# Optimization experiments

Hardware: AMD Instinct MI355X
Metric: run time of the kernel (lower is better)

The kernel has to match this reference:

```python
import jax, jax.numpy as jnp
import numpy as np

IN_F = 256
OUT_F = 256
H = 4
DH = OUT_F // H  # 64
N = 6144


def setup_inputs() -> dict:
    key = jax.random.key(0)
    ks = jax.random.split(key, 6)
    x = jax.random.normal(ks[0], (N, IN_F), dtype=jnp.float32)
    adj = jax.random.randint(ks[1], (N, N), 0, 2, dtype=jnp.int32)
    # per-head Linear(in_features, d_head): weights [H, IN_F, DH], bias [H, DH]
    W = jax.random.normal(ks[2], (H, IN_F, DH), dtype=jnp.float32) / np.sqrt(IN_F)
    Wb = jax.random.normal(ks[3], (H, DH), dtype=jnp.float32) * 0.01
    # per-head Linear(2*d_head, 1): weights [H, 2*DH], bias [H]
    A = jax.random.normal(ks[4], (H, 2 * DH), dtype=jnp.float32) / np.sqrt(2 * DH)
    Ab = jax.random.normal(ks[5], (H,), dtype=jnp.float32) * 0.01
    return {"x": x, "adj": adj, "W": W, "Wb": Wb, "A": A, "Ab": Ab}


def reference(x, adj, W, Wb, A, Ab):
    # h[h,n,d] = per-head linear projection of node features
    h = jnp.einsum("ni,hid->hnd", x, W) + Wb[:, None, :]
    a_src, a_dst = A[:, :DH], A[:, DH:]
    # score(i,j) = a_src . h_i + a_dst . h_j + b  (decomposed concat-linear)
    s_src = jnp.einsum("hnd,hd->hn", h, a_src) + Ab[:, None]  # [H, N]
    s_dst = jnp.einsum("hnd,hd->hn", h, a_dst)                # [H, N]
    scores = s_src[:, :, None] + s_dst[:, None, :]            # [H, N, N]
    # Faithful to source: non-edges get score 0.0 (not -inf) before softmax
    scores = jnp.where(adj[None, :, :] > 0, scores, 0.0)
    probs = jax.nn.softmax(scores, axis=-1)                   # row softmax
    out = jnp.einsum("hij,hjd->hid", probs, h)                # [H, N, DH]
    # concat heads along feature dim -> [N, H*DH]
    return jnp.transpose(out, (1, 0, 2)).reshape(N, H * DH)
```

## Files before the change

kernel.cpp:

```cpp
#include <hip/hip_runtime.h>
#include <stdint.h>

#define NN 6144
#define NC 576

typedef float f32x4 __attribute__((ext_vector_type(4)));
typedef __bf16 bf16x8v __attribute__((ext_vector_type(8)));

__device__ __forceinline__ unsigned short f2bf(float f) {
  unsigned u = __float_as_uint(f);
  u += 0x7FFFu + ((u >> 16) & 1u);
  return (unsigned short)(u >> 16);
}

__device__ __forceinline__ float bf2f(unsigned short s) {
  unsigned u = (unsigned)s << 16;
  return __uint_as_float(u);
}

__device__ __forceinline__ unsigned char f2e4m3(float f) {
  unsigned u = __float_as_uint(f);
  unsigned sgn = (u >> 24) & 0x80u;
  unsigned au = u & 0x7FFFFFFFu;
  if (au >= 0x43E00000u) return (unsigned char)(sgn | 0x7E);
  if (au < 0x3C800000u) {
    int q = (int)rintf(__uint_as_float(au) * 512.0f);
    return (unsigned char)(sgn | (q >= 8 ? 0x08 : q));
  }
  unsigned r = au + 0x7FFFFu + ((au >> 20) & 1u);
  int e = (int)(r >> 23) - 127;
  unsigned m = (r >> 20) & 7u;
  return (unsigned char)(sgn | ((unsigned)(e + 7) << 3) | m);
}

__device__ __forceinline__ unsigned short pack2(float a, float b) {
  return (unsigned short)f2e4m3(a) | ((unsigned short)f2e4m3(b) << 8);
}

__device__ __forceinline__ void async_load16(const void* g, void* l) {
  __builtin_amdgcn_global_load_lds(
      (__attribute__((address_space(1))) void*)(uintptr_t)g,
      (__attribute__((address_space(3))) void*)(uint32_t)(uintptr_t)l,
      16, 0, 0);
}

__global__ __launch_bounds__(256) void p0s(
    const float* __restrict__ W,
    const float* __restrict__ Aw, const float* __restrict__ Wb,
    unsigned short* __restrict__ wsw, float* __restrict__ Acat,
    float* __restrict__ T)
{
  const int bid = blockIdx.x, t = threadIdx.x;
  if (bid < 8) {
#pragma unroll
    for (int i = 0; i < 4; ++i) {
      const int e = bid * 256 + t + i * 2048;
      const int l = e & 63, kc = (e >> 6) & 7, ct = e >> 9;
      const int c = ct * 16 + (l & 15);
      const int h = c >> 6, d0 = c & 63;
      const int ks = kc * 32 + (l >> 4) * 8;
      const float* src = W + h * 16384 + ks * 64 + d0;
      unsigned uu[4];
#pragma unroll
      for (int j = 0; j < 4; ++j)
        uu[j] = (unsigned)f2bf(src[(2*j) * 64]) | ((unsigned)f2bf(src[(2*j+1) * 64]) << 16);
      *(uint4*)(wsw + (size_t)e * 8) = (uint4){uu[0], uu[1], uu[2], uu[3]};
    }
    return;
  }
  T[t] = 0.f;
  const int h = t >> 6, d = t & 63;
  Acat[t]       = Aw[h * 128 + d];
  Acat[256 + t] = Aw[h * 128 + 64 + d];
  Acat[512 + t] = Wb[t];
}

__global__ __launch_bounds__(256) void k1m(
    const float* __restrict__ x, const unsigned short* __restrict__ wsw,
    const float* __restrict__ Acat, const float* __restrict__ Ab,
    const int* __restrict__ adj, unsigned* __restrict__ bm,
    unsigned char* __restrict__ V8, float* __restrict__ e_src, float* __restrict__ T)
{
  __shared__ unsigned char lsh[16384];
  __shared__ float lt[256];
  const int t = threadIdx.x;

  if (blockIdx.x >= 192) {
    const int pb = blockIdx.x - 192;
    const int4* src = (const int4*)adj + (size_t)pb * 2048;
    unsigned char* ln = lsh;
#pragma unroll
    for (int i = 0; i < 8; ++i) {
      int4 q = src[t + i * 256];
      unsigned nib = (unsigned)q.x | ((unsigned)q.y << 1) |
                     ((unsigned)q.z << 2) | ((unsigned)q.w << 3);
      ln[t + i * 256] = (unsigned char)nib;
    }
    __syncthreads();
    const uint2 b2 = *(const uint2*)(ln + t * 8);
    unsigned pl = (b2.x | (b2.x >> 4)) & 0x00FF00FFu; pl = (pl | (pl >> 8)) & 0xFFFFu;
    unsigned ph = (b2.y | (b2.y >> 4)) & 0x00FF00FFu; ph = (ph | (ph >> 8)) & 0xFFFFu;
    bm[pb * 256 + t] = pl | (ph << 16);
    return;
  }

  const int w = t >> 6, l = t & 63;
  const int v = blockIdx.x * 4 + w;
  const int mt = v >> 1, nh = v & 1;
  const int i0 = mt * 16, c0 = nh * 128;
  const int lm = l & 15, lk = l >> 4;

  {
    unsigned short* lx = (unsigned short*)lsh;
    const float* xb = x + (size_t)(blockIdx.x * 32) * 256;
#pragma unroll
    for (int j = 0; j < 4; ++j) {
      const int e = t + j * 256;
      const int tile = e >> 9, e9 = e & 511;
      const int el = e9 & 63, kc = e9 >> 6;
      const int node = tile * 16 + (el & 15);
      const int ks = kc * 32 + (el >> 4) * 8;
      const float4* xp = (const float4*)(xb + (size_t)node * 256 + ks);
      float4 v0 = xp[0], v1 = xp[1];
      uint4 o;
      o.x = (unsigned)f2bf(v0.x) | ((unsigned)f2bf(v0.y) << 16);
      o.y = (unsigned)f2bf(v0.z) | ((unsigned)f2bf(v0.w) << 16);
      o.z = (unsigned)f2bf(v1.x) | ((unsigned)f2bf(v1.y) << 16);
      o.w = (unsigned)f2bf(v1.z) | ((unsigned)f2bf(v1.w) << 16);
      *(uint4*)(lx + (size_t)e * 8) = o;
    }
  }
  lt[t] = 0.f;
  __syncthreads();

  f32x4 acc[8];
#pragma unroll
  for (int nt = 0; nt < 8; ++nt) acc[nt] = (f32x4){0.f, 0.f, 0.f, 0.f};

  const unsigned short* ap = (const unsigned short*)lsh + (((size_t)(w >> 1)) * 512 + l) * 8;
  const unsigned short* bp = wsw + ((size_t)nh * 4096 + l) * 8;

#pragma unroll
  for (int kc = 0; kc < 8; ++kc) {
    bf16x8v a = *(const bf16x8v*)(ap + (size_t)kc * 512);
#pragma unroll
    for (int nt = 0; nt < 8; ++nt) {
      bf16x8v b = *(const bf16x8v*)(bp + ((size_t)nt * 512 + kc * 64) * 8);
      acc[nt] = __builtin_amdgcn_mfma_f32_16x16x32_bf16(a, b, acc[nt], 0, 0, 0);
    }
  }

  float asv[8], adv[8];
#pragma unroll
  for (int nt = 0; nt < 8; ++nt) {
    const int cc = c0 + nt * 16 + lm;
    const float wb = Acat[512 + cc];
#pragma unroll
    for (int rr = 0; rr < 4; ++rr) acc[nt][rr] += wb;
    asv[nt] = Acat[cc];
    adv[nt] = Acat[256 + cc];
  }

#pragma unroll
  for (int nt = 0; nt < 8; ++nt)
    atomicAdd(&lt[c0 + nt * 16 + lm], acc[nt][0] + acc[nt][1] + acc[nt][2] + acc[nt][3]);

  float ss[2][4], sd[2][4];
#pragma unroll
  for (int hl = 0; hl < 2; ++hl)
#pragma unroll
    for (int rr = 0; rr < 4; ++rr) {
      float s1 = 0.f, s2 = 0.f;
#pragma unroll
      for (int j = 0; j < 4; ++j) {
        s1 += acc[hl * 4 + j][rr] * asv[hl * 4 + j];
        s2 += acc[hl * 4 + j][rr] * adv[hl * 4 + j];
      }
      ss[hl][rr] = s1; sd[hl][rr] = s2;
    }
#pragma unroll
  for (int off = 1; off < 16; off <<= 1)
#pragma unroll
    for (int hl = 0; hl < 2; ++hl)
#pragma unroll
      for (int rr = 0; rr < 4; ++rr) {
        ss[hl][rr] += __shfl_xor(ss[hl][rr], off);
        sd[hl][rr] += __shfl_xor(sd[hl][rr], off);
      }

  float ed[2][4];
#pragma unroll
  for (int hl = 0; hl < 2; ++hl)
#pragma unroll
    for (int rr = 0; rr < 4; ++rr) ed[hl][rr] = expf(sd[hl][rr]);

  if (lm == 0) {
#pragma unroll
    for (int hl = 0; hl < 2; ++hl) {
      const int hh = nh * 2 + hl;
      const float ab = Ab[hh];
#pragma unroll
      for (int rr = 0; rr < 4; ++rr)
        e_src[(size_t)hh * NN + i0 + lk * 4 + rr] = expf(ss[hl][rr] + ab);
    }
  }

  __syncthreads();

  unsigned char* mylv = lsh + w * 4096;
#pragma unroll
  for (int nt = 0; nt < 8; ++nt) {
    const int hl = nt >> 2;
    const int d = (nt & 3) * 16 + lm;
    const int lcE = hl * 128 + d;
    const int lcP = lcE + 64;
    *(unsigned short*)(mylv + lcE * 16 + lk * 4)     = pack2(ed[hl][0] * acc[nt][0], ed[hl][1] * acc[nt][1]);
    *(unsigned short*)(mylv + lcE * 16 + lk * 4 + 2) = pack2(ed[hl][2] * acc[nt][2], ed[hl][3] * acc[nt][3]);
    *(unsigned short*)(mylv + lcP * 16 + lk * 4)     = pack2(acc[nt][0], acc[nt][1]);
    *(unsigned short*)(mylv + lcP * 16 + lk * 4 + 2) = pack2(acc[nt][2], acc[nt][3]);
  }
#pragma unroll
  for (int j = 0; j < 4; ++j) {
    const int lc = j * 64 + l;
    uint4 val = *(const uint4*)(mylv + lc * 16);
    *(uint4*)(V8 + (size_t)(nh * 256 + lc) * NN + i0) = val;
  }
  if (lm == 0) {
#pragma unroll
    for (int hl = 0; hl < 2; ++hl) {
      const int hh = nh * 2 + hl;
      unsigned char* pq = V8 + (size_t)(512 + hh) * NN + i0 + lk * 4;
      *(unsigned short*)pq       = pack2(ed[hl][0], ed[hl][1]);
      *(unsigned short*)(pq + 2) = pack2(ed[hl][2], ed[hl][3]);
    }
    if (nh == 0)
      *(unsigned*)(V8 + (size_t)516 * NN + i0 + lk * 4) = 0x38383838u;
  }

  __syncthreads();
  atomicAdd(&T[t], lt[t]);
}

__global__ __launch_bounds__(256, 3) void k2_gemm(
    const unsigned* __restrict__ bm, const unsigned char* __restrict__ V8,
    unsigned short* __restrict__ out2b, float* __restrict__ out2e, int nks)
{
  __shared__ unsigned char lB[2][144 * 128];
  const int t   = threadIdx.x;
  const int ks  = blockIdx.x / 192;
  const int r   = blockIdx.x - ks * 192;
  const int cb  = r & 3;
  const int rb  = r >> 2;
  const int krange = NN / nks;
  const int i0 = rb * 128, n0 = cb * 144, k0 = ks * krange;
  const int w = t >> 6, l = t & 63;
  const int lm = l & 15, lk = l >> 4;

  f32x4 acc[2][9];
#pragma unroll
  for (int mt = 0; mt < 2; ++mt)
#pragma unroll
    for (int nt = 0; nt < 9; ++nt) acc[mt][nt] = (f32x4){0.f, 0.f, 0.f, 0.f};

  int scol[5], sgr[5];
#pragma unroll
  for (int u = 0; u < 5; ++u) {
    const int gi = u * 256 + t;
    scol[u] = gi >> 3;
    sgr[u]  = (gi & 7) ^ (scol[u] & 7);
  }
  const int dbase4 = (1024 + (t & ~63)) * 16;

  const unsigned* gA0 = bm + (size_t)(i0 + w * 32 + lm) * (NN / 32) + (k0 >> 5) + lk;
  const unsigned char* gBb = V8 + (size_t)n0 * NN + k0;

  const int iters = krange / 128;

#define K2_STAGE(BUF, IT)                                                        \
  do {                                                                           \
    const unsigned char* gB = gBb + (IT) * 128;                                  \
    _Pragma("unroll")                                                            \
    for (int u = 0; u < 4; ++u)                                                  \
      async_load16(gB + (size_t)scol[u] * NN + sgr[u] * 16,                      \
                   (char*)lB[BUF] + (size_t)(u * 256 + (t & ~63)) * 16);         \
    if (t < 128)                                                                 \
      async_load16(gB + (size_t)scol[4] * NN + sgr[4] * 16,                      \
                   (char*)lB[BUF] + dbase4);                                     \
  } while (0)

  unsigned bits_c[2], bits_n[2];
  K2_STAGE(0, 0);
#pragma unroll
  for (int mt = 0; mt < 2; ++mt) bits_c[mt] = gA0[(size_t)mt * 16 * (NN / 32)];
  __syncthreads();

  int cur = 0;
  for (int it = 0; it < iters; ++it) {
    if (it + 1 < iters) {
      K2_STAGE(cur ^ 1, it + 1);
#pragma unroll
      for (int mt = 0; mt < 2; ++mt)
        bits_n[mt] = gA0[(size_t)mt * 16 * (NN / 32) + (it + 1) * 4];
    }

    longlong2 afr[2][2];
#pragma unroll
    for (int mt = 0; mt < 2; ++mt) {
      unsigned u[8];
#pragma unroll
      for (int i = 0; i < 8; ++i) {
        unsigned nib = (bits_c[mt] >> (4 * i)) & 0xFu;
        u[i] = ((nib * 0x00204081u) & 0x01010101u) << 3;
      }
      afr[mt][0].x = (long long)(((unsigned long long)u[1] << 32) | u[0]);
      afr[mt][0].y = (long long)(((unsigned long long)u[3] << 32) | u[2]);
      afr[mt][1].x = (long long)(((unsigned long long)u[5] << 32) | u[4]);
      afr[mt][1].y = (long long)(((unsigned long long)u[7] << 32) | u[6]);
    }

#pragma unroll
    for (int b = 0; b < 2; ++b) {
#pragma unroll
      for (int nt = 0; nt < 9; ++nt) {
        const int cc = nt * 16 + lm;
        const int pos = (lk * 2 + b) ^ (cc & 7);
        longlong2 bv = *(const longlong2*)(lB[cur] + cc * 128 + pos * 16);
#pragma unroll
        for (int mt = 0; mt < 2; ++mt) {
          acc[mt][nt] = __builtin_amdgcn_mfma_f32_16x16x32_fp8_fp8(
              afr[mt][b].x, bv.x, acc[mt][nt], 0, 0, 0);
          acc[mt][nt] = __builtin_amdgcn_mfma_f32_16x16x32_fp8_fp8(
              afr[mt][b].y, bv.y, acc[mt][nt], 0, 0, 0);
        }
      }
    }

    if (it + 1 < iters) {
#pragma unroll
      for (int mt = 0; mt < 2; ++mt) bits_c[mt] = bits_n[mt];
    }
    __syncthreads();
    cur ^= 1;
  }
#undef K2_STAGE

  unsigned short* lw = (unsigned short*)((char*)lB[0] + w * 4608);
  float* oe = out2e + (size_t)ks * ((size_t)NN * 64);
  unsigned short* pb = out2b + ((size_t)(ks * 4 + cb) * NN + i0 + w * 32) * 144;
#pragma unroll
  for (int mt = 0; mt < 2; ++mt) {
#pragma unroll
    for (int nt = 0; nt < 9; ++nt) {
      const int coll = nt * 16 + lm;
#pragma unroll
      for (int rr = 0; rr < 4; ++rr)
        lw[(lk * 4 + rr) * 144 + coll] = f2bf(acc[mt][nt][rr] * 64.0f);
      if (cb == 3 && nt >= 5) {
        const int row = i0 + w * 32 + mt * 16 + lk * 4;
#pragma unroll
        for (int rr = 0; rr < 4; ++rr)
          oe[(size_t)(row + rr) * 64 + (n0 + coll - 512)] = acc[mt][nt][rr] * 64.0f;
      }
    }
    const uint4* ls = (const uint4*)((char*)lB[0] + w * 4608);
    char* dst = (char*)(pb + (size_t)mt * 16 * 144);
    for (int s = l; s < 288; s += 64)
      *(uint4*)(dst + s * 16) = ls[s];
  }
}

__global__ __launch_bounds__(256) void k3_final(
    const unsigned short* __restrict__ out2b, const float* __restrict__ out2e,
    const float* __restrict__ e_src, const float* __restrict__ T,
    float* __restrict__ out, int nks)
{
  const int n = blockIdx.x, c = threadIdx.x;
  const int h = c >> 6, d = c & 63;
  const int cS = h * 128 + d, cP = cS + 64;
  const int cbS = cS / 144, ofS = cS % 144;
  const int cbP = cP / 144, ofP = cP % 144;
  float Se = 0.f, Sp = 0.f, E = 0.f, dg = 0.f;
  for (int s = 0; s < nks; ++s) {
    const unsigned short* base = out2b + (size_t)s * 4 * NN * 144;
    Se += bf2f(base[((size_t)cbS * NN + n) * 144 + ofS]);
    Sp += bf2f(base[((size_t)cbP * NN + n) * 144 + ofP]);
    const float* re = out2e + (size_t)s * NN * 64 + (size_t)n * 64;
    E  += re[h];
    dg += re[4];
  }
  float e = e_src[h * NN + n];
  float D = e * E + ((float)NN - dg);
  out[(size_t)n * 256 + c] = (e * Se + (T[c] - Sp)) / D;
}

extern "C" void kernel_launch(void* const* d_in, const int* in_sizes, int n_in,
                              void* d_out, int out_size, void* d_ws, size_t ws_size,
                              hipStream_t stream) {
  const float* x  = (const float*)d_in[0];
  const int*   adj= (const int*)d_in[1];
  const float* W  = (const float*)d_in[2];
  const float* Wb = (const float*)d_in[3];
  const float* Aw = (const float*)d_in[4];
  const float* Ab = (const float*)d_in[5];
  float* out = (float*)d_out;
  char* ws = (char*)d_ws;
  unsigned char* V8 = (unsigned char*)ws;
  float* e_src = (float*)(ws + 3538944);
  float* T     = (float*)(ws + 3637248);
  float* Acat  = (float*)(ws + 3638272);
  unsigned short* wsw = (unsigned short*)(ws + 3641344);
  unsigned* bm = (unsigned*)(ws + 6918144);
  unsigned short* out2b = (unsigned short*)(ws + 44666880);
  float* out2e = (float*)(ws + 87134208);

  const size_t slabB = (size_t)4 * NN * 144 * 2;
  const size_t slabE = (size_t)NN * 64 * 4;
  int nks = 2;
  if (ws_size >= 44666880 + 4 * slabB + 4 * slabE)  nks = 4;

  hipLaunchKernelGGL(p0s, dim3(9), dim3(256), 0, stream,
                     W, Aw, Wb, wsw, Acat, T);
  hipLaunchKernelGGL(k1m, dim3(4800), dim3(256), 0, stream,
                     x, wsw, Acat, Ab, adj, bm, V8, e_src, T);
  hipLaunchKernelGGL(k2_gemm, dim3(192 * nks), dim3(256), 0, stream, bm, V8, out2b, out2e, nks);
  hipLaunchKernelGGL(k3_final, dim3(NN), dim3(256), 0, stream, out2b, out2e, e_src, T, out, nks);
}
```

Before: 271.5 us.

## Split k2 GEMM loads into phases interleaved with MFMA via fine-grained waitcnt barriers

Restructures the k2_gemm main loop into three MFMA phases of three N-tiles each. The next stage's async global-to-LDS loads are issued in chunks between phases, and explicit vmcnt waits plus s_barrier replace the single per-iteration __syncthreads. s_setprio raises wave priority during MFMA bursts. The intent is to overlap load issue with compute and shorten barrier stalls. In exchange, LDS padding grows to 160 rows so all threads issue the fifth load unconditionally, which uses more shared memory and may reduce occupancy. The hand-tuned waitcnt counts are fragile.

```diff
diff --git a/kernel.cpp b/kernel.cpp
--- a/kernel.cpp
+++ b/kernel.cpp
@@ -245,7 +245,7 @@
     const unsigned* __restrict__ bm, const unsigned char* __restrict__ V8,
     unsigned short* __restrict__ out2b, float* __restrict__ out2e, int nks)
 {
-  __shared__ unsigned char lB[2][144 * 128];
+  __shared__ unsigned char lB[2][160 * 128];
   const int t   = threadIdx.x;
   const int ks  = blockIdx.x / 192;
   const int r   = blockIdx.x - ks * 192;
@@ -269,80 +269,120 @@
     scol[u] = gi >> 3;
     sgr[u]  = (gi & 7) ^ (scol[u] & 7);
   }
-  const int dbase4 = (1024 + (t & ~63)) * 16;
 
   const unsigned* gA0 = bm + (size_t)(i0 + w * 32 + lm) * (NN / 32) + (k0 >> 5) + lk;
   const unsigned char* gBb = V8 + (size_t)n0 * NN + k0;
 
   const int iters = krange / 128;
 
-#define K2_STAGE(BUF, IT)                                                        \
-  do {                                                                           \
-    const unsigned char* gB = gBb + (IT) * 128;                                  \
-    _Pragma("unroll")                                                            \
-    for (int u = 0; u < 4; ++u)                                                  \
-      async_load16(gB + (size_t)scol[u] * NN + sgr[u] * 16,                      \
-                   (char*)lB[BUF] + (size_t)(u * 256 + (t & ~63)) * 16);         \
-    if (t < 128)                                                                 \
-      async_load16(gB + (size_t)scol[4] * NN + sgr[4] * 16,                      \
-                   (char*)lB[BUF] + dbase4);                                     \
+#define K2_ISSUE(U)                                                             \
+  async_load16(gBn + (size_t)scol[U] * NN + sgr[U] * 16,                        \
+               dst + (size_t)((U) * 256 + (t & ~63)) * 16)
+
+#define K2_EXPAND                                                               \
+  do {                                                                          \
+    unsigned bits[2] = {bc0, bc1};                                              \
+    _Pragma("unroll")                                                           \
+    for (int mtq = 0; mtq < 2; ++mtq) {                                         \
+      unsigned u[8];                                                            \
+      _Pragma("unroll")                                                         \
+      for (int i = 0; i < 8; ++i) {                                             \
+        unsigned nib = (bits[mtq] >> (4 * i)) & 0xFu;                           \
+        u[i] = ((nib * 0x00204081u) & 0x01010101u) << 3;                        \
+      }                                                                         \
+      afr[mtq][0].x = (long long)(((unsigned long long)u[1] << 32) | u[0]);     \
+      afr[mtq][0].y = (long long)(((unsigned long long)u[3] << 32) | u[2]);     \
+      afr[mtq][1].x = (long long)(((unsigned long long)u[5] << 32) | u[4]);     \
+      afr[mtq][1].y = (long long)(((unsigned long long)u[7] << 32) | u[6]);     \
+    }                                                                           \
   } while (0)
 
-  unsigned bits_c[2], bits_n[2];
-  K2_STAGE(0, 0);
-#pragma unroll
-  for (int mt = 0; mt < 2; ++mt) bits_c[mt] = gA0[(size_t)mt * 16 * (NN / 32)];
+#define K2_MFMA_PHASE(NTB)                                                      \
+  __builtin_amdgcn_s_setprio(1);                                                \
+  _Pragma("unroll")                                                             \
+  for (int b2 = 0; b2 < 2; ++b2) {                                              \
+    _Pragma("unroll")                                                           \
+    for (int q = 0; q < 3; ++q) {                                               \
+      const int cc = ((NTB) + q) * 16 + lm;                                     \
+      const int pos = (lk * 2 + b2) ^ (cc & 7);                                 \
+      longlong2 bv = *(const longlong2*)(lB[cur] + cc * 128 + pos * 16);        \
+      _Pragma("unroll")                                                         \
+      for (int mtq = 0; mtq < 2; ++mtq) {                                       \
+        acc[mtq][(NTB) + q] = __builtin_amdgcn_mfma_f32_16x16x32_fp8_fp8(       \
+            afr[mtq][b2].x, bv.x, acc[mtq][(NTB) + q], 0, 0, 0);                \
+        acc[mtq][(NTB) + q] = __builtin_amdgcn_mfma_f32_16x16x32_fp8_fp8(       \
+            afr[mtq][b2].y, bv.y, acc[mtq][(NTB) + q], 0, 0, 0);                \
+      }                                                                         \
+    }                                                                           \
+  }                                                                             \
+  __builtin_amdgcn_s_setprio(0)
+
+  unsigned bc0 = gA0[0];
+  unsigned bc1 = gA0[16 * (NN / 32)];
+  {
+    const unsigned char* gBn = gBb;
+    unsigned char* dst = (unsigned char*)lB[0];
+#pragma unroll
+    for (int u = 0; u < 5; ++u) { K2_ISSUE(u); }
+  }
+  asm volatile("s_waitcnt vmcnt(0)" ::: "memory");
   __syncthreads();
 
   int cur = 0;
-  for (int it = 0; it < iters; ++it) {
-    if (it + 1 < iters) {
-      K2_STAGE(cur ^ 1, it + 1);
-#pragma unroll
-      for (int mt = 0; mt < 2; ++mt)
-        bits_n[mt] = gA0[(size_t)mt * 16 * (NN / 32) + (it + 1) * 4];
-    }
-
+  for (int it = 0; it < iters - 1; ++it) {
+    const unsigned char* gBn = gBb + (it + 1) * 128;
+    unsigned char* dst = (unsigned char*)lB[cur ^ 1];
     longlong2 afr[2][2];
-#pragma unroll
-    for (int mt = 0; mt < 2; ++mt) {
-      unsigned u[8];
-#pragma unroll
-      for (int i = 0; i < 8; ++i) {
-        unsigned nib = (bits_c[mt] >> (4 * i)) & 0xFu;
-        u[i] = ((nib * 0x00204081u) & 0x01010101u) << 3;
-      }
-      afr[mt][0].x = (long long)(((unsigned long long)u[1] << 32) | u[0]);
-      afr[mt][0].y = (long long)(((unsigned long long)u[3] << 32) | u[2]);
-      afr[mt][1].x = (long long)(((unsigned long long)u[5] << 32) | u[4]);
-      afr[mt][1].y = (long long)(((unsigned long long)u[7] << 32) | u[6]);
-    }
-
-#pragma unroll
-    for (int b = 0; b < 2; ++b) {
-#pragma unroll
-      for (int nt = 0; nt < 9; ++nt) {
-        const int cc = nt * 16 + lm;
-        const int pos = (lk * 2 + b) ^ (cc & 7);
-        longlong2 bv = *(const longlong2*)(lB[cur] + cc * 128 + pos * 16);
-#pragma unroll
-        for (int mt = 0; mt < 2; ++mt) {
-          acc[mt][nt] = __builtin_amdgcn_mfma_f32_16x16x32_fp8_fp8(
-              afr[mt][b].x, bv.x, acc[mt][nt], 0, 0, 0);
-          acc[mt][nt] = __builtin_amdgcn_mfma_f32_16x16x32_fp8_fp8(
-              afr[mt][b].y, bv.y, acc[mt][nt], 0, 0, 0);
-        }
-      }
-    }
-
-    if (it + 1 < iters) {
-#pragma unroll
-      for (int mt = 0; mt < 2; ++mt) bits_c[mt] = bits_n[mt];
-    }
-    __syncthreads();
+
+    asm volatile("s_waitcnt vmcnt(3)" ::: "memory");
+    __builtin_amdgcn_s_barrier();
+    __builtin_amdgcn_sched_barrier(0);
+    unsigned bn0 = gA0[(size_t)(it + 1) * 4];
+    unsigned bn1 = gA0[16 * (NN / 32) + (size_t)(it + 1) * 4];
+    K2_ISSUE(0);
+    K2_ISSUE(1);
+    K2_EXPAND;
+    K2_MFMA_PHASE(0);
+
+    asm volatile("s_waitcnt vmcnt(6)" ::: "memory");
+    __builtin_amdgcn_s_barrier();
+    __builtin_amdgcn_sched_barrier(0);
+    K2_ISSUE(2);
+    K2_ISSUE(3);
+    K2_MFMA_PHASE(3);
+
+    asm volatile("s_waitcnt vmcnt(6)" ::: "memory");
+    __builtin_amdgcn_s_barrier();
+    __builtin_amdgcn_sched_barrier(0);
+    K2_ISSUE(4);
+    K2_MFMA_PHASE(6);
+
+    bc0 = bn0; bc1 = bn1;
     cur ^= 1;
   }
-#undef K2_STAGE
+
+  {
+    longlong2 afr[2][2];
+    asm volatile("s_waitcnt vmcnt(3)" ::: "memory");
+    __builtin_amdgcn_s_barrier();
+    __builtin_amdgcn_sched_barrier(0);
+    K2_EXPAND;
+    K2_MFMA_PHASE(0);
+
+    asm volatile("s_waitcnt vmcnt(2)" ::: "memory");
+    __builtin_amdgcn_s_barrier();
+    __builtin_amdgcn_sched_barrier(0);
+    K2_MFMA_PHASE(3);
+
+    asm volatile("s_waitcnt vmcnt(0)" ::: "memory");
+    __builtin_amdgcn_s_barrier();
+    __builtin_amdgcn_sched_barrier(0);
+    K2_MFMA_PHASE(6);
+  }
+#undef K2_ISSUE
+#undef K2_EXPAND
+#undef K2_MFMA_PHASE
+  __syncthreads();
 
   unsigned short* lw = (unsigned short*)((char*)lB[0] + w * 4608);
   float* oe = out2e + (size_t)ks * ((size_t)NN * 64);
@@ -363,9 +403,9 @@
       }
     }
     const uint4* ls = (const uint4*)((char*)lB[0] + w * 4608);
-    char* dst = (char*)(pb + (size_t)mt * 16 * 144);
+    char* dst2 = (char*)(pb + (size_t)mt * 16 * 144);
     for (int s = l; s < 288; s += 64)
-      *(uint4*)(dst + s * 16) = ls[s];
+      *(uint4*)(dst2 + s * 16) = ls[s];
   }
 }
 
```

New measurement: 275.4 us. About the same (+1.4%).
